# Optimization experiments

Measured on AMD Instinct MI355X. Metric: run time of the kernel, lower is better.

## Reference

```python
import jax, jax.numpy as jnp
import numpy as np

N = 50000       # num nodes
E = 800000      # num edges (before self loops)
D_IN = 128
D_H = 128
D_OUT = 40


def setup_inputs() -> dict:
    key = jax.random.key(0)
    ks = jax.random.split(key, 8)
    x = jax.random.normal(ks[0], (N, D_IN), dtype=jnp.float32)
    edge_index = jax.random.randint(ks[1], (2, E), 0, N, dtype=jnp.int32)
    # GCNConv weights (glorot-ish scale) and biases
    W1 = jax.random.normal(ks[2], (D_IN, D_H), dtype=jnp.float32) / np.sqrt(D_IN)
    b1 = jnp.zeros((D_H,), dtype=jnp.float32)
    W2 = jax.random.normal(ks[3], (D_H, D_H), dtype=jnp.float32) / np.sqrt(D_H)
    b2 = jnp.zeros((D_H,), dtype=jnp.float32)
    Wc = jax.random.normal(ks[4], (D_H, D_OUT), dtype=jnp.float32) / np.sqrt(D_H)
    bc = jnp.zeros((D_OUT,), dtype=jnp.float32)
    return {"x": x, "edge_index": edge_index, "W1": W1, "b1": b1,
            "W2": W2, "b2": b2, "Wc": Wc, "bc": bc}


def _gcn_conv(x, row, col, num_nodes, W, b):
    # PyG GCNConv: h = X @ W; out[c] += norm(r,c) * h[r]; out += b
    h = x @ W
    deg = jax.ops.segment_sum(jnp.ones(row.shape[0], h.dtype), col,
                              num_segments=num_nodes)
    dinv = jnp.where(deg > 0, jax.lax.rsqrt(deg), 0.0).astype(h.dtype)
    norm = dinv[row] * dinv[col]                      # [E+N]
    msg = h[row] * norm[:, None]                      # gather + scale
    agg = jax.ops.segment_sum(msg, col, num_segments=num_nodes)  # scatter-add
    return agg + b


def reference(x, edge_index, W1, b1, W2, b2, Wc, bc):
    # add self loops (GCNConv default add_self_loops=True)
    loops = jnp.arange(N, dtype=edge_index.dtype)
    row = jnp.concatenate([edge_index[0], loops])
    col = jnp.concatenate([edge_index[1], loops])
    h = jax.nn.relu(_gcn_conv(x, row, col, N, W1, b1))
    h = jax.nn.relu(_gcn_conv(h, row, col, N, W2, b2))
    g = jnp.mean(h, axis=0)                           # mean pool over nodes
    return g @ Wc + bc                                # [D_OUT]
```

## Files before the change

### kernel.cpp

```cpp
#include <hip/hip_runtime.h>
#include <hip/hip_fp16.h>


typedef _Float16 half8 __attribute__((ext_vector_type(8)));
typedef float f32x4 __attribute__((ext_vector_type(4)));
typedef float f32x2 __attribute__((ext_vector_type(2)));

constexpr int N = 50000;
constexpr int E = 800000;
constexpr int D = 128;
constexpr int DOUT = 40;
constexpr int CAP = 64;
constexpr int HB = 128;
constexpr int EPB = E / HB;
constexpr int HWRD = 12500;
constexpr int GM = (N + 127) / 128;
constexpr int NW = N / 4;
constexpr int GF = 3 * GM;

__global__ __launch_bounds__(1024) void k_hist(const int* __restrict__ col,
                                               unsigned char* __restrict__ hist,
                                               unsigned char* __restrict__ rank,
                                               const float* __restrict__ W1,
                                               const float* __restrict__ W2,
                                               __half* __restrict__ T1,
                                               __half* __restrict__ T2) {
    __shared__ unsigned int h[HWRD];
    int b = blockIdx.x, t = threadIdx.x;
    if (b >= HB) {
        int o = (b - HB) * 1024 + t;
        const float* W = (o < 16384) ? W1 : W2;
        __half* T = (o < 16384) ? T1 : T2;
        int oo = o & 16383;
        int n = oo >> 7, k = oo & 127;
        T[oo] = (__half)W[k * 128 + n];
        return;
    }
    for (int i = t; i < HWRD; i += 1024) h[i] = 0;
    __syncthreads();
    int e0 = b * EPB;
    for (int e = e0 + t; e < e0 + EPB; e += 1024) {
        int c = col[e];
        unsigned int old = atomicAdd(&h[c >> 2], 1u << ((c & 3) * 8));
        rank[e] = (unsigned char)((old >> ((c & 3) * 8)) & 0xff);
    }
    __syncthreads();
    unsigned int* out = (unsigned int*)(hist + (size_t)b * 50000);
    for (int i = t; i < HWRD; i += 1024) out[i] = h[i];
}

__global__ void k_colscan(unsigned char* __restrict__ hist, int* __restrict__ deg,
                          float* __restrict__ dinv) {
    int c4 = blockIdx.x * 256 + threadIdx.x;
    if (c4 >= HWRD) return;
    unsigned int* hw = (unsigned int*)hist;
    unsigned int run = 0;
#pragma unroll 8
    for (int b = 0; b < HB; ++b) {
        unsigned int v = hw[b * HWRD + c4];
        hw[b * HWRD + c4] = run;
        run += v;
    }
#pragma unroll
    for (int j = 0; j < 4; ++j) {
        int dg = (run >> (8 * j)) & 0xff;
        deg[4 * c4 + j] = dg;
        dinv[4 * c4 + j] = rsqrtf((float)(dg + 1));
    }
}

__device__ __forceinline__ unsigned char f8enc(float v) {
    return (unsigned char)(__builtin_amdgcn_cvt_pk_fp8_f32(v, v, 0, false) & 0xff);
}
__device__ __forceinline__ void add8f8(f32x2* a, uint2 u) {
    a[0] += __builtin_amdgcn_cvt_pk_f32_fp8(u.x, false);
    a[1] += __builtin_amdgcn_cvt_pk_f32_fp8(u.x, true);
    a[2] += __builtin_amdgcn_cvt_pk_f32_fp8(u.y, false);
    a[3] += __builtin_amdgcn_cvt_pk_f32_fp8(u.y, true);
}

__device__ __forceinline__ half8 ldA(const float* rowp, int koff) {
    float4 u0 = *(const float4*)(rowp + koff);
    float4 u1 = *(const float4*)(rowp + koff + 4);
    half8 r;
    r[0] = (_Float16)u0.x; r[1] = (_Float16)u0.y;
    r[2] = (_Float16)u0.z; r[3] = (_Float16)u0.w;
    r[4] = (_Float16)u1.x; r[5] = (_Float16)u1.y;
    r[6] = (_Float16)u1.z; r[7] = (_Float16)u1.w;
    return r;
}
__device__ __forceinline__ half8 ldA(const __half* rowp, int koff) {
    return *(const half8*)(rowp + koff);
}

template <typename TA>
__device__ __forceinline__ void mfma_gemm(const TA* __restrict__ A,
                                          const __half* __restrict__ Wt,
                                          const float* __restrict__ dinv,
                                          unsigned char* __restrict__ out8,
                                          int row0, int tid) {
    int wave = tid >> 6, lane = tid & 63;
    int quad = lane >> 4, c16 = lane & 15;
    int m0 = row0 + wave * 32;
    int ra = m0 + c16;      if (ra >= N) ra = 0;
    int rb = m0 + 16 + c16; if (rb >= N) rb = 0;
    const TA* pa = A + (size_t)ra * D;
    const TA* pb = A + (size_t)rb * D;

    f32x4 acc[2][8];
#pragma unroll
    for (int i = 0; i < 2; ++i)
#pragma unroll
        for (int j = 0; j < 8; ++j) acc[i][j] = (f32x4){0.f, 0.f, 0.f, 0.f};

#pragma unroll
    for (int kq = 0; kq < 4; ++kq) {
        int koff = kq * 32 + quad * 8;
        half8 a0 = ldA(pa, koff);
        half8 a1 = ldA(pb, koff);
#pragma unroll
        for (int nt = 0; nt < 8; ++nt) {
            half8 bf = *(const half8*)(Wt + (size_t)(nt * 16 + c16) * D + koff);
            acc[0][nt] = __builtin_amdgcn_mfma_f32_16x16x32_f16(a0, bf, acc[0][nt], 0, 0, 0);
            acc[1][nt] = __builtin_amdgcn_mfma_f32_16x16x32_f16(a1, bf, acc[1][nt], 0, 0, 0);
        }
    }

#pragma unroll
    for (int rt = 0; rt < 2; ++rt) {
        int mt = m0 + rt * 16;
#pragma unroll
        for (int i = 0; i < 4; ++i) {
            int grow = mt + quad * 4 + i;
            if (grow < N) {
                float s = dinv[grow];
                unsigned char* orow = out8 + (size_t)grow * D + c16;
#pragma unroll
                for (int nt = 0; nt < 8; ++nt)
                    orow[nt * 16] = f8enc(acc[rt][nt][i] * s);
            }
        }
    }
}

__global__ __launch_bounds__(256) void k_fuse(const int* __restrict__ ei,
                                              const unsigned char* __restrict__ hist,
                                              const unsigned char* __restrict__ rank,
                                              unsigned short* __restrict__ csr,
                                              const float* __restrict__ x,
                                              const __half* __restrict__ Wt1,
                                              const float* __restrict__ dinv,
                                              unsigned char* __restrict__ out8) {
    int b = blockIdx.x, m = b % 3;
    if (m < 2) {
        int sb = (b / 3) * 2 + m;
        int e0 = sb * 1024 + threadIdx.x * 4;
        if (e0 >= E) return;
        int4 rr = *(const int4*)(ei + e0);
        int4 cc = *(const int4*)(ei + E + e0);
        uchar4 kk = *(const uchar4*)(rank + e0);
        int rs[4] = {rr.x, rr.y, rr.z, rr.w};
        int cs[4] = {cc.x, cc.y, cc.z, cc.w};
        int ks[4] = {kk.x, kk.y, kk.z, kk.w};
#pragma unroll
        for (int i = 0; i < 4; ++i) {
            int e = e0 + i;
            int c = cs[i];
            int chunk = e / EPB;
            int slot = (int)hist[(size_t)chunk * 50000 + c] + ks[i];
            if (slot < CAP) csr[(c << 6) + slot] = (unsigned short)rs[i];
        }
        return;
    }
    mfma_gemm<float>(x, Wt1, dinv, out8, (b / 3) * 128, threadIdx.x);
}

__device__ __forceinline__ float agg_core(int c, int lane,
                                          const unsigned char* __restrict__ hs8,
                                          const int* __restrict__ deg,
                                          const unsigned short* __restrict__ csr,
                                          float* __restrict__ a0out) {
    int qw = lane >> 4;
    int q  = lane & 15;
    int dgRaw = deg[c];
    int dg = dgRaw < CAP ? dgRaw : CAP;
    float dc = rsqrtf((float)(dgRaw + 1));
    int e0 = c << 6;

    f32x2 a0[4], a1[4], a2[4], a3[4];
#pragma unroll
    for (int i = 0; i < 4; ++i) {
        a0[i] = (f32x2){0.f, 0.f}; a1[i] = (f32x2){0.f, 0.f};
        a2[i] = (f32x2){0.f, 0.f}; a3[i] = (f32x2){0.f, 0.f};
    }
    if (qw == 0)
        add8f8(a0, *(const uint2*)&hs8[((unsigned)c << 7) + q * 8]);

    int j = 0;
    for (; j + 16 <= dg; j += 16) {
        int r0 = csr[e0 + j + qw];
        int r1 = csr[e0 + j + 4 + qw];
        int r2 = csr[e0 + j + 8 + qw];
        int r3 = csr[e0 + j + 12 + qw];
        uint2 u0 = *(const uint2*)&hs8[((unsigned)r0 << 7) + q * 8];
        uint2 u1 = *(const uint2*)&hs8[((unsigned)r1 << 7) + q * 8];
        uint2 u2 = *(const uint2*)&hs8[((unsigned)r2 << 7) + q * 8];
        uint2 u3 = *(const uint2*)&hs8[((unsigned)r3 << 7) + q * 8];
        add8f8(a0, u0); add8f8(a1, u1); add8f8(a2, u2); add8f8(a3, u3);
    }
    if (j + 8 <= dg) {
        int r0 = csr[e0 + j + qw];
        int r1 = csr[e0 + j + 4 + qw];
        uint2 u0 = *(const uint2*)&hs8[((unsigned)r0 << 7) + q * 8];
        uint2 u1 = *(const uint2*)&hs8[((unsigned)r1 << 7) + q * 8];
        add8f8(a0, u0); add8f8(a1, u1);
        j += 8;
    }
    if (j + 4 <= dg) {
        int r0 = csr[e0 + j + qw];
        add8f8(a0, *(const uint2*)&hs8[((unsigned)r0 << 7) + q * 8]);
        j += 4;
    }
    int rem = dg - j;
    if (qw < rem) {
        int r0 = csr[e0 + j + qw];
        add8f8(a1, *(const uint2*)&hs8[((unsigned)r0 << 7) + q * 8]);
    }

#pragma unroll
    for (int i = 0; i < 4; ++i) { a0[i] += a1[i]; a2[i] += a3[i]; a0[i] += a2[i]; }
#pragma unroll
    for (int t = 0; t < 8; ++t) {
        float v = a0[t >> 1][t & 1];
        v += __shfl_xor(v, 16, 64);
        v += __shfl_xor(v, 32, 64);
        a0out[t] = v;
    }
    return dc;
}

__global__ __launch_bounds__(256) void k_agg1(const unsigned char* __restrict__ hs8,
                                              const int* __restrict__ deg,
                                              const unsigned short* __restrict__ csr,
                                              const float* __restrict__ bias,
                                              __half* __restrict__ outH) {
    int wave = threadIdx.x >> 6;
    int lane = threadIdx.x & 63;
    int c = blockIdx.x * 4 + wave;
    float a0[8];
    float dc = agg_core(c, lane, hs8, deg, csr, a0);
    if ((lane >> 4) == 0) {
        int q = lane & 15;
        union { __half2 h[4]; uint4 u; } p;
#pragma unroll
        for (int i = 0; i < 4; ++i) {
            float xv = fmaxf(fmaf(dc, a0[2 * i],     bias[q * 8 + 2 * i]),     0.f);
            float yv = fmaxf(fmaf(dc, a0[2 * i + 1], bias[q * 8 + 2 * i + 1]), 0.f);
            p.h[i] = __floats2half2_rn(xv, yv);
        }
        *(uint4*)&outH[(size_t)c * D + q * 8] = p.u;
    }
}

__global__ __launch_bounds__(256) void k_gemm(const __half* __restrict__ A,
                                              const __half* __restrict__ Wt,
                                              const float* __restrict__ dinv,
                                              unsigned char* __restrict__ out8) {
    mfma_gemm<__half>(A, Wt, dinv, out8, blockIdx.x * 128, threadIdx.x);
}

__global__ __launch_bounds__(256) void k_agg2(const unsigned char* __restrict__ hs8,
                                              const int* __restrict__ deg,
                                              const unsigned short* __restrict__ csr,
                                              const float* __restrict__ bias,
                                              float* __restrict__ gpart) {
    __shared__ float gblk[4][128];
    int wave = threadIdx.x >> 6;
    int lane = threadIdx.x & 63;
    int c = blockIdx.x * 4 + wave;
    float a0[8];
    float dc = agg_core(c, lane, hs8, deg, csr, a0);
    if ((lane >> 4) == 0) {
        int q = lane & 15;
#pragma unroll
        for (int i = 0; i < 8; ++i)
            gblk[wave][q * 8 + i] = fmaxf(fmaf(dc, a0[i], bias[q * 8 + i]), 0.f);
    }
    __syncthreads();
    int t = threadIdx.x;
    if (t < 128)
        gpart[(size_t)blockIdx.x * 128 + t] =
            gblk[0][t] + gblk[1][t] + gblk[2][t] + gblk[3][t];
}

__global__ __launch_bounds__(256) void k_pool(const float* __restrict__ gpart,
                                              float* __restrict__ gpart2) {
    int d = threadIdx.x & 127;
    int half = threadIdx.x >> 7;
    int b = blockIdx.x;
    int per = (NW + 255) / 256;
    int r0 = b * per;
    int r1 = r0 + per;
    if (r1 > NW) r1 = NW;
    float acc = 0.f;
    for (int r = r0 + half; r < r1; r += 2)
        acc += gpart[(size_t)r * D + d];
    __shared__ float red[256];
    red[threadIdx.x] = acc;
    __syncthreads();
    if (half == 0) gpart2[(size_t)b * D + d] = red[d] + red[128 + d];
}

__global__ __launch_bounds__(512) void k_final(const float* __restrict__ gpart2,
                                               const float* __restrict__ Wc,
                                               const float* __restrict__ bc,
                                               float* __restrict__ out) {
    __shared__ float g[D];
    __shared__ float red[512];
    int t = threadIdx.x;
    int d = t & 127, grp = t >> 7;
    float s = 0.f;
#pragma unroll 4
    for (int w = grp * 64; w < grp * 64 + 64; ++w)
        s += gpart2[(size_t)w * D + d];
    red[t] = s;
    __syncthreads();
    if (grp == 0)
        g[d] = (red[d] + red[128 + d] + red[256 + d] + red[384 + d]) * (1.0f / (float)N);
    __syncthreads();
    if (t < DOUT) {
        float acc = bc[t];
        for (int dd = 0; dd < D; ++dd) acc = fmaf(g[dd], Wc[dd * DOUT + t], acc);
        out[t] = acc;
    }
}

extern "C" void kernel_launch(void* const* d_in, const int* in_sizes, int n_in,
                              void* d_out, int out_size, void* d_ws, size_t ws_size,
                              hipStream_t stream) {
    const float* x  = (const float*)d_in[0];
    const int*   ei = (const int*)d_in[1];
    const float* W1 = (const float*)d_in[2];
    const float* b1 = (const float*)d_in[3];
    const float* W2 = (const float*)d_in[4];
    const float* b2 = (const float*)d_in[5];
    const float* Wc = (const float*)d_in[6];
    const float* bc = (const float*)d_in[7];
    float* out = (float*)d_out;

    char* ws = (char*)d_ws;
    size_t off = 0;
    auto alloc = [&](size_t bytes) {
        void* p = ws + off;
        off += (bytes + 511) & ~(size_t)511;
        return p;
    };
    unsigned char*  hist   = (unsigned char*) alloc((size_t)HB * 50000);
    unsigned char*  rank   = (unsigned char*) alloc((size_t)E);
    int*            deg    = (int*)           alloc((size_t)N * 4);
    float*          dinv   = (float*)         alloc((size_t)N * 4);
    unsigned short* csr    = (unsigned short*)alloc((size_t)N * CAP * 2);
    unsigned char*  hs8    = (unsigned char*) alloc((size_t)N * D);
    __half*         hactH  = (__half*)        alloc((size_t)N * D * 2);
    __half*         Wt1    = (__half*)        alloc((size_t)D * D * 2);
    __half*         Wt2    = (__half*)        alloc((size_t)D * D * 2);
    float*          gpart  = (float*)         alloc((size_t)NW * D * 4);
    float*          gpart2 = (float*)         alloc((size_t)256 * D * 4);
    (void)ws_size; (void)in_sizes; (void)n_in; (void)out_size;

    const int* col = ei + E;

    k_hist<<<HB + 32, 1024, 0, stream>>>(col, hist, rank, W1, W2, Wt1, Wt2);
    k_colscan<<<(HWRD + 255) / 256, 256, 0, stream>>>(hist, deg, dinv);
    k_fuse<<<GF, 256, 0, stream>>>(ei, hist, rank, csr, x, Wt1, dinv, hs8);

    k_agg1<<<NW, 256, 0, stream>>>(hs8, deg, csr, b1, hactH);
    k_gemm<<<GM, 256, 0, stream>>>(hactH, Wt2, dinv, hs8);
    k_agg2<<<NW, 256, 0, stream>>>(hs8, deg, csr, b2, gpart);
    k_pool<<<256, 256, 0, stream>>>(gpart, gpart2);
    k_final<<<1, 512, 0, stream>>>(gpart2, Wc, bc, out);
}
```

Baseline: 208.6 us.

## Parallelize column scan across four waves and widen edge parallelism in aggregation

The column scan now splits the 128 histogram chunks across four waves per column group, loading 32 values each, combining partial sums through shared memory, then writing exclusive prefixes. This shortens the serial dependent-load chain per thread. The aggregation core now uses 8 edge lanes by 8 feature lanes and processes the 128-wide row in two 64-byte halves. That doubles concurrent edge gathers per wave at the cost of narrower per-row loads, two passes over the CSR indices and an extra shuffle stage.

```diff
diff --git a/kernel.cpp b/kernel.cpp
--- a/kernel.cpp
+++ b/kernel.cpp
@@ -49,23 +49,41 @@
     for (int i = t; i < HWRD; i += 1024) out[i] = h[i];
 }
 
-__global__ void k_colscan(unsigned char* __restrict__ hist, int* __restrict__ deg,
-                          float* __restrict__ dinv) {
-    int c4 = blockIdx.x * 256 + threadIdx.x;
-    if (c4 >= HWRD) return;
+__global__ __launch_bounds__(256) void k_colscan(unsigned char* __restrict__ hist,
+                                                 int* __restrict__ deg,
+                                                 float* __restrict__ dinv) {
+    __shared__ unsigned int part[4][64];
     unsigned int* hw = (unsigned int*)hist;
-    unsigned int run = 0;
-#pragma unroll 8
-    for (int b = 0; b < HB; ++b) {
-        unsigned int v = hw[b * HWRD + c4];
-        hw[b * HWRD + c4] = run;
-        run += v;
-    }
-#pragma unroll
-    for (int j = 0; j < 4; ++j) {
-        int dg = (run >> (8 * j)) & 0xff;
-        deg[4 * c4 + j] = dg;
-        dinv[4 * c4 + j] = rsqrtf((float)(dg + 1));
+    int c4 = blockIdx.x * 64 + (threadIdx.x & 63);
+    int qq = threadIdx.x >> 6;
+    bool ok = c4 < HWRD;
+    unsigned int v[32];
+    unsigned int s = 0;
+    if (ok) {
+#pragma unroll
+        for (int i = 0; i < 32; ++i) v[i] = hw[(size_t)(qq * 32 + i) * HWRD + c4];
+#pragma unroll
+        for (int i = 0; i < 32; ++i) s += v[i];
+    }
+    part[qq][threadIdx.x & 63] = s;
+    __syncthreads();
+    unsigned int base = 0;
+    for (int k = 0; k < qq; ++k) base += part[k][threadIdx.x & 63];
+    if (ok) {
+        unsigned int run = base;
+#pragma unroll
+        for (int i = 0; i < 32; ++i) {
+            hw[(size_t)(qq * 32 + i) * HWRD + c4] = run;
+            run += v[i];
+        }
+        if (qq == 3) {
+#pragma unroll
+            for (int j = 0; j < 4; ++j) {
+                int dg = (run >> (8 * j)) & 0xff;
+                deg[4 * c4 + j] = dg;
+                dinv[4 * c4 + j] = rsqrtf((float)(dg + 1));
+            }
+        }
     }
 }
 
@@ -180,61 +198,66 @@
                                           const int* __restrict__ deg,
                                           const unsigned short* __restrict__ csr,
                                           float* __restrict__ a0out) {
-    int qw = lane >> 4;
-    int q  = lane & 15;
+    int qw = lane >> 3;
+    int q  = lane & 7;
     int dgRaw = deg[c];
     int dg = dgRaw < CAP ? dgRaw : CAP;
     float dc = rsqrtf((float)(dgRaw + 1));
     int e0 = c << 6;
 
-    f32x2 a0[4], a1[4], a2[4], a3[4];
-#pragma unroll
-    for (int i = 0; i < 4; ++i) {
-        a0[i] = (f32x2){0.f, 0.f}; a1[i] = (f32x2){0.f, 0.f};
-        a2[i] = (f32x2){0.f, 0.f}; a3[i] = (f32x2){0.f, 0.f};
-    }
-    if (qw == 0)
-        add8f8(a0, *(const uint2*)&hs8[((unsigned)c << 7) + q * 8]);
-
-    int j = 0;
-    for (; j + 16 <= dg; j += 16) {
-        int r0 = csr[e0 + j + qw];
-        int r1 = csr[e0 + j + 4 + qw];
-        int r2 = csr[e0 + j + 8 + qw];
-        int r3 = csr[e0 + j + 12 + qw];
-        uint2 u0 = *(const uint2*)&hs8[((unsigned)r0 << 7) + q * 8];
-        uint2 u1 = *(const uint2*)&hs8[((unsigned)r1 << 7) + q * 8];
-        uint2 u2 = *(const uint2*)&hs8[((unsigned)r2 << 7) + q * 8];
-        uint2 u3 = *(const uint2*)&hs8[((unsigned)r3 << 7) + q * 8];
-        add8f8(a0, u0); add8f8(a1, u1); add8f8(a2, u2); add8f8(a3, u3);
-    }
-    if (j + 8 <= dg) {
-        int r0 = csr[e0 + j + qw];
-        int r1 = csr[e0 + j + 4 + qw];
-        uint2 u0 = *(const uint2*)&hs8[((unsigned)r0 << 7) + q * 8];
-        uint2 u1 = *(const uint2*)&hs8[((unsigned)r1 << 7) + q * 8];
-        add8f8(a0, u0); add8f8(a1, u1);
-        j += 8;
-    }
-    if (j + 4 <= dg) {
-        int r0 = csr[e0 + j + qw];
-        add8f8(a0, *(const uint2*)&hs8[((unsigned)r0 << 7) + q * 8]);
-        j += 4;
-    }
-    int rem = dg - j;
-    if (qw < rem) {
-        int r0 = csr[e0 + j + qw];
-        add8f8(a1, *(const uint2*)&hs8[((unsigned)r0 << 7) + q * 8]);
-    }
-
-#pragma unroll
-    for (int i = 0; i < 4; ++i) { a0[i] += a1[i]; a2[i] += a3[i]; a0[i] += a2[i]; }
-#pragma unroll
-    for (int t = 0; t < 8; ++t) {
-        float v = a0[t >> 1][t & 1];
-        v += __shfl_xor(v, 16, 64);
-        v += __shfl_xor(v, 32, 64);
-        a0out[t] = v;
+#pragma unroll 1
+    for (int h = 0; h < 2; ++h) {
+        int boff = h * 64 + q * 8;
+        f32x2 a0[4], a1[4], a2[4], a3[4];
+#pragma unroll
+        for (int i = 0; i < 4; ++i) {
+            a0[i] = (f32x2){0.f, 0.f}; a1[i] = (f32x2){0.f, 0.f};
+            a2[i] = (f32x2){0.f, 0.f}; a3[i] = (f32x2){0.f, 0.f};
+        }
+        if (qw == 0)
+            add8f8(a0, *(const uint2*)&hs8[((unsigned)c << 7) + boff]);
+
+        int j = 0;
+        for (; j + 32 <= dg; j += 32) {
+            int r0 = csr[e0 + j + qw];
+            int r1 = csr[e0 + j + 8 + qw];
+            int r2 = csr[e0 + j + 16 + qw];
+            int r3 = csr[e0 + j + 24 + qw];
+            uint2 u0 = *(const uint2*)&hs8[((unsigned)r0 << 7) + boff];
+            uint2 u1 = *(const uint2*)&hs8[((unsigned)r1 << 7) + boff];
+            uint2 u2 = *(const uint2*)&hs8[((unsigned)r2 << 7) + boff];
+            uint2 u3 = *(const uint2*)&hs8[((unsigned)r3 << 7) + boff];
+            add8f8(a0, u0); add8f8(a1, u1); add8f8(a2, u2); add8f8(a3, u3);
+        }
+        if (j + 16 <= dg) {
+            int r0 = csr[e0 + j + qw];
+            int r1 = csr[e0 + j + 8 + qw];
+            uint2 u0 = *(const uint2*)&hs8[((unsigned)r0 << 7) + boff];
+            uint2 u1 = *(const uint2*)&hs8[((unsigned)r1 << 7) + boff];
+            add8f8(a0, u0); add8f8(a1, u1);
+            j += 16;
+        }
+        if (j + 8 <= dg) {
+            int r0 = csr[e0 + j + qw];
+            add8f8(a0, *(const uint2*)&hs8[((unsigned)r0 << 7) + boff]);
+            j += 8;
+        }
+        int rem = dg - j;
+        if (qw < rem) {
+            int r0 = csr[e0 + j + qw];
+            add8f8(a1, *(const uint2*)&hs8[((unsigned)r0 << 7) + boff]);
+        }
+
+#pragma unroll
+        for (int i = 0; i < 4; ++i) { a0[i] += a1[i]; a2[i] += a3[i]; a0[i] += a2[i]; }
+#pragma unroll
+        for (int t = 0; t < 8; ++t) {
+            float v = a0[t >> 1][t & 1];
+            v += __shfl_xor(v, 8, 64);
+            v += __shfl_xor(v, 16, 64);
+            v += __shfl_xor(v, 32, 64);
+            a0out[h * 8 + t] = v;
+        }
     }
     return dc;
 }
@@ -247,18 +270,22 @@
     int wave = threadIdx.x >> 6;
     int lane = threadIdx.x & 63;
     int c = blockIdx.x * 4 + wave;
-    float a0[8];
+    float a0[16];
     float dc = agg_core(c, lane, hs8, deg, csr, a0);
-    if ((lane >> 4) == 0) {
-        int q = lane & 15;
-        union { __half2 h[4]; uint4 u; } p;
-#pragma unroll
-        for (int i = 0; i < 4; ++i) {
-            float xv = fmaxf(fmaf(dc, a0[2 * i],     bias[q * 8 + 2 * i]),     0.f);
-            float yv = fmaxf(fmaf(dc, a0[2 * i + 1], bias[q * 8 + 2 * i + 1]), 0.f);
-            p.h[i] = __floats2half2_rn(xv, yv);
-        }
-        *(uint4*)&outH[(size_t)c * D + q * 8] = p.u;
+    if (lane < 8) {
+        int q = lane;
+#pragma unroll
+        for (int h = 0; h < 2; ++h) {
+            union { __half2 hh[4]; uint4 u; } p;
+#pragma unroll
+            for (int i = 0; i < 4; ++i) {
+                int ch = h * 64 + q * 8 + 2 * i;
+                float xv = fmaxf(fmaf(dc, a0[h * 8 + 2 * i],     bias[ch]),     0.f);
+                float yv = fmaxf(fmaf(dc, a0[h * 8 + 2 * i + 1], bias[ch + 1]), 0.f);
+                p.hh[i] = __floats2half2_rn(xv, yv);
+            }
+            *(uint4*)&outH[(size_t)c * D + h * 64 + q * 8] = p.u;
+        }
     }
 }
 
@@ -278,13 +305,17 @@
     int wave = threadIdx.x >> 6;
     int lane = threadIdx.x & 63;
     int c = blockIdx.x * 4 + wave;
-    float a0[8];
+    float a0[16];
     float dc = agg_core(c, lane, hs8, deg, csr, a0);
-    if ((lane >> 4) == 0) {
-        int q = lane & 15;
-#pragma unroll
-        for (int i = 0; i < 8; ++i)
-            gblk[wave][q * 8 + i] = fmaxf(fmaf(dc, a0[i], bias[q * 8 + i]), 0.f);
+    if (lane < 8) {
+        int q = lane;
+#pragma unroll
+        for (int h = 0; h < 2; ++h)
+#pragma unroll
+            for (int i = 0; i < 8; ++i) {
+                int ch = h * 64 + q * 8 + i;
+                gblk[wave][ch] = fmaxf(fmaf(dc, a0[h * 8 + i], bias[ch]), 0.f);
+            }
     }
     __syncthreads();
     int t = threadIdx.x;
@@ -371,7 +402,7 @@
     const int* col = ei + E;
 
     k_hist<<<HB + 32, 1024, 0, stream>>>(col, hist, rank, W1, W2, Wt1, Wt2);
-    k_colscan<<<(HWRD + 255) / 256, 256, 0, stream>>>(hist, deg, dinv);
+    k_colscan<<<(HWRD + 63) / 64, 256, 0, stream>>>(hist, deg, dinv);
     k_fuse<<<GF, 256, 0, stream>>>(ei, hist, rank, csr, x, Wt1, dinv, hs8);
 
     k_agg1<<<NW, 256, 0, stream>>>(hs8, deg, csr, b1, hactH);
```

Measured after the change: 260.9 us. 25.0% more time.

## Store layer-1 activations as fp8 and parallelize column scan across blocks

Applied to the files above, without the earlier changes.

The layer-1 aggregation output is now written as fp8 bytes instead of fp16, and the second GEMM decodes fp8 to fp16 on load, halving the intermediate activation traffic. Separately, the histogram column prefix scan is split into four 32-bucket segments per column, combined through shared memory, so more threads participate and each loads its values up front. The fp8 activation adds quantization error before the second layer and extra conversion instructions in the GEMM load path.

```diff
diff --git a/kernel.cpp b/kernel.cpp
--- a/kernel.cpp
+++ b/kernel.cpp
@@ -49,23 +49,41 @@
     for (int i = t; i < HWRD; i += 1024) out[i] = h[i];
 }
 
-__global__ void k_colscan(unsigned char* __restrict__ hist, int* __restrict__ deg,
-                          float* __restrict__ dinv) {
-    int c4 = blockIdx.x * 256 + threadIdx.x;
-    if (c4 >= HWRD) return;
+__global__ __launch_bounds__(256) void k_colscan(unsigned char* __restrict__ hist,
+                                                 int* __restrict__ deg,
+                                                 float* __restrict__ dinv) {
+    __shared__ unsigned int part[4][64];
     unsigned int* hw = (unsigned int*)hist;
-    unsigned int run = 0;
-#pragma unroll 8
-    for (int b = 0; b < HB; ++b) {
-        unsigned int v = hw[b * HWRD + c4];
-        hw[b * HWRD + c4] = run;
-        run += v;
-    }
-#pragma unroll
-    for (int j = 0; j < 4; ++j) {
-        int dg = (run >> (8 * j)) & 0xff;
-        deg[4 * c4 + j] = dg;
-        dinv[4 * c4 + j] = rsqrtf((float)(dg + 1));
+    int c4 = blockIdx.x * 64 + (threadIdx.x & 63);
+    int qq = threadIdx.x >> 6;
+    bool ok = c4 < HWRD;
+    unsigned int v[32];
+    unsigned int s = 0;
+    if (ok) {
+#pragma unroll
+        for (int i = 0; i < 32; ++i) v[i] = hw[(size_t)(qq * 32 + i) * HWRD + c4];
+#pragma unroll
+        for (int i = 0; i < 32; ++i) s += v[i];
+    }
+    part[qq][threadIdx.x & 63] = s;
+    __syncthreads();
+    unsigned int base = 0;
+    for (int k = 0; k < qq; ++k) base += part[k][threadIdx.x & 63];
+    if (ok) {
+        unsigned int run = base;
+#pragma unroll
+        for (int i = 0; i < 32; ++i) {
+            hw[(size_t)(qq * 32 + i) * HWRD + c4] = run;
+            run += v[i];
+        }
+        if (qq == 3) {
+#pragma unroll
+            for (int j = 0; j < 4; ++j) {
+                int dg = (run >> (8 * j)) & 0xff;
+                deg[4 * c4 + j] = dg;
+                dinv[4 * c4 + j] = rsqrtf((float)(dg + 1));
+            }
+        }
     }
 }
 
@@ -89,8 +107,18 @@
     r[6] = (_Float16)u1.z; r[7] = (_Float16)u1.w;
     return r;
 }
-__device__ __forceinline__ half8 ldA(const __half* rowp, int koff) {
-    return *(const half8*)(rowp + koff);
+__device__ __forceinline__ half8 ldA(const unsigned char* rowp, int koff) {
+    uint2 u = *(const uint2*)(rowp + koff);
+    f32x2 f0 = __builtin_amdgcn_cvt_pk_f32_fp8(u.x, false);
+    f32x2 f1 = __builtin_amdgcn_cvt_pk_f32_fp8(u.x, true);
+    f32x2 f2 = __builtin_amdgcn_cvt_pk_f32_fp8(u.y, false);
+    f32x2 f3 = __builtin_amdgcn_cvt_pk_f32_fp8(u.y, true);
+    half8 r;
+    r[0] = (_Float16)f0[0]; r[1] = (_Float16)f0[1];
+    r[2] = (_Float16)f1[0]; r[3] = (_Float16)f1[1];
+    r[4] = (_Float16)f2[0]; r[5] = (_Float16)f2[1];
+    r[6] = (_Float16)f3[0]; r[7] = (_Float16)f3[1];
+    return r;
 }
 
 template <typename TA>
@@ -243,7 +271,7 @@
                                               const int* __restrict__ deg,
                                               const unsigned short* __restrict__ csr,
                                               const float* __restrict__ bias,
-                                              __half* __restrict__ outH) {
+                                              unsigned char* __restrict__ out8) {
     int wave = threadIdx.x >> 6;
     int lane = threadIdx.x & 63;
     int c = blockIdx.x * 4 + wave;
@@ -251,22 +279,19 @@
     float dc = agg_core(c, lane, hs8, deg, csr, a0);
     if ((lane >> 4) == 0) {
         int q = lane & 15;
-        union { __half2 h[4]; uint4 u; } p;
-#pragma unroll
-        for (int i = 0; i < 4; ++i) {
-            float xv = fmaxf(fmaf(dc, a0[2 * i],     bias[q * 8 + 2 * i]),     0.f);
-            float yv = fmaxf(fmaf(dc, a0[2 * i + 1], bias[q * 8 + 2 * i + 1]), 0.f);
-            p.h[i] = __floats2half2_rn(xv, yv);
-        }
-        *(uint4*)&outH[(size_t)c * D + q * 8] = p.u;
-    }
-}
-
-__global__ __launch_bounds__(256) void k_gemm(const __half* __restrict__ A,
+        union { unsigned char b[8]; uint2 u; } p;
+#pragma unroll
+        for (int i = 0; i < 8; ++i)
+            p.b[i] = f8enc(fmaxf(fmaf(dc, a0[i], bias[q * 8 + i]), 0.f));
+        *(uint2*)&out8[((unsigned)c << 7) + q * 8] = p.u;
+    }
+}
+
+__global__ __launch_bounds__(256) void k_gemm(const unsigned char* __restrict__ A,
                                               const __half* __restrict__ Wt,
                                               const float* __restrict__ dinv,
                                               unsigned char* __restrict__ out8) {
-    mfma_gemm<__half>(A, Wt, dinv, out8, blockIdx.x * 128, threadIdx.x);
+    mfma_gemm<unsigned char>(A, Wt, dinv, out8, blockIdx.x * 128, threadIdx.x);
 }
 
 __global__ __launch_bounds__(256) void k_agg2(const unsigned char* __restrict__ hs8,
@@ -361,7 +386,7 @@
     float*          dinv   = (float*)         alloc((size_t)N * 4);
     unsigned short* csr    = (unsigned short*)alloc((size_t)N * CAP * 2);
     unsigned char*  hs8    = (unsigned char*) alloc((size_t)N * D);
-    __half*         hactH  = (__half*)        alloc((size_t)N * D * 2);
+    unsigned char*  h18    = (unsigned char*) alloc((size_t)N * D);
     __half*         Wt1    = (__half*)        alloc((size_t)D * D * 2);
     __half*         Wt2    = (__half*)        alloc((size_t)D * D * 2);
     float*          gpart  = (float*)         alloc((size_t)NW * D * 4);
@@ -371,11 +396,11 @@
     const int* col = ei + E;
 
     k_hist<<<HB + 32, 1024, 0, stream>>>(col, hist, rank, W1, W2, Wt1, Wt2);
-    k_colscan<<<(HWRD + 255) / 256, 256, 0, stream>>>(hist, deg, dinv);
+    k_colscan<<<(HWRD + 63) / 64, 256, 0, stream>>>(hist, deg, dinv);
     k_fuse<<<GF, 256, 0, stream>>>(ei, hist, rank, csr, x, Wt1, dinv, hs8);
 
-    k_agg1<<<NW, 256, 0, stream>>>(hs8, deg, csr, b1, hactH);
-    k_gemm<<<GM, 256, 0, stream>>>(hactH, Wt2, dinv, hs8);
+    k_agg1<<<NW, 256, 0, stream>>>(hs8, deg, csr, b1, h18);
+    k_gemm<<<GM, 256, 0, stream>>>(h18, Wt2, dinv, hs8);
     k_agg2<<<NW, 256, 0, stream>>>(hs8, deg, csr, b2, gpart);
     k_pool<<<256, 256, 0, stream>>>(gpart, gpart2);
     k_final<<<1, 512, 0, stream>>>(gpart2, Wc, bc, out);
```

New measurement: 206.3 us, median of 2. No clear change (-1.1%).
